# Performance work log

Hardware: AMD Instinct MI355X
Metric: run time of the kernel (lower is better)

## Reference

```python
import jax, jax.numpy as jnp
import numpy as np
jax.config.update("jax_enable_x64", True)  # hash math needs int64 like torch .long()

NUM_LEVELS = 16
BASE_RES = 16
LOG2_HASHMAP = 19
FEAT_DIM = 2
N_POINTS = 2097152
PRIMES = (1, 2654435761, 805459861)


def setup_inputs() -> dict:
    key = jax.random.key(0)
    k1, k2 = jax.random.split(key)
    xyz = jax.random.uniform(k1, (N_POINTS, 3), dtype=jnp.float32)
    # 16 hash tables of shape [2**19, 2], init randn * 0.1 as in the module
    tables = jax.random.normal(
        k2, (NUM_LEVELS, 2 ** LOG2_HASHMAP, FEAT_DIM), dtype=jnp.float32) * 0.1
    return {"xyz": xyz, "tables": tables}


def reference(xyz, tables):
    L, F = NUM_LEVELS, FEAT_DIM
    N = xyz.shape[0]
    grid_res = (BASE_RES * (2 ** jnp.arange(L, dtype=jnp.int64)))  # [L]
    # scale + truncate-to-int per level (xyz >= 0 so trunc == floor, matches .long())
    scaled = xyz[None, :, :] * grid_res[:, None, None].astype(xyz.dtype)  # [L, N, 3]
    idx = scaled.astype(jnp.int64)  # [L, N, 3]
    # spatial hash: (x*1) ^ (y*p1) ^ (z*p2) mod 2**19
    h = (idx[..., 0] * PRIMES[0]) ^ (idx[..., 1] * PRIMES[1]) ^ (idx[..., 2] * PRIMES[2])
    h = h % (1 << LOG2_HASHMAP)  # [L, N], non-negative
    # per-level gather from its own table
    feats = jax.vmap(lambda t, hh: t[hh])(tables, h)  # [L, N, F]
    # concat level features along last dim -> [N, L*F]
    return jnp.transpose(feats, (1, 0, 2)).reshape(N, L * F)
```

## Files before the change

### kernel.cpp

```cpp
#include <hip/hip_runtime.h>

#define NUM_LEVELS 16
#define LOG2_HASHMAP 19
#define TABLE_SIZE (1u << LOG2_HASHMAP)

typedef unsigned long long u64;

__global__ __launch_bounds__(256) void gather_kernel(
    const float* __restrict__ xyz,
    const float* __restrict__ tables,
    u64* __restrict__ ws,
    int n_points, int blocks_per_level)
{
    int b = blockIdx.x;
    int l = b / blocks_per_level;
    int n = (b - l * blocks_per_level) * 256 + threadIdx.x;
    if (n >= n_points) return;

    float x = xyz[n * 3 + 0];
    float y = xyz[n * 3 + 1];
    float z = xyz[n * 3 + 2];

    float res = (float)(16u << l);
    unsigned ix = (unsigned)(x * res);
    unsigned iy = (unsigned)(y * res);
    unsigned iz = (unsigned)(z * res);
    unsigned h = (ix ^ (iy * 2654435761u) ^ (iz * 805459861u)) & (TABLE_SIZE - 1u);

    u64 f = *((const u64*)tables + (((size_t)l << LOG2_HASHMAP) + h));
    __builtin_nontemporal_store(f, ws + (size_t)l * n_points + n);
}

__global__ __launch_bounds__(256) void transpose_kernel(
    const u64* __restrict__ ws,
    u64* __restrict__ out,
    int n_points)
{
    __shared__ u64 tile[128][NUM_LEVELS + 1];
    int n0 = blockIdx.x * 128;

    for (int i = threadIdx.x; i < 128 * NUM_LEVELS; i += 256) {
        int l = i >> 7;
        int n = i & 127;
        int gn = n0 + n;
        u64 v = (gn < n_points)
                  ? __builtin_nontemporal_load(ws + (size_t)l * n_points + gn)
                  : 0ull;
        tile[n][l] = v;
    }
    __syncthreads();

    for (int i = threadIdx.x; i < 128 * NUM_LEVELS; i += 256) {
        int n = i >> 4;
        int l = i & 15;
        if (n0 + n < n_points)
            __builtin_nontemporal_store(tile[n][l], out + (size_t)n0 * NUM_LEVELS + i);
    }
}

__global__ __launch_bounds__(256) void fused_kernel(
    const float* __restrict__ xyz,
    const float* __restrict__ tables,
    u64* __restrict__ out,
    int n_points)
{
    int tid = blockIdx.x * blockDim.x + threadIdx.x;
    int n = tid >> 4;
    int l = tid & 15;
    if (n >= n_points) return;
    float x = xyz[n * 3 + 0], y = xyz[n * 3 + 1], z = xyz[n * 3 + 2];
    float res = (float)(16u << l);
    unsigned ix = (unsigned)(x * res);
    unsigned iy = (unsigned)(y * res);
    unsigned iz = (unsigned)(z * res);
    unsigned h = (ix ^ (iy * 2654435761u) ^ (iz * 805459861u)) & (TABLE_SIZE - 1u);
    u64 f = *((const u64*)tables + (((size_t)l << LOG2_HASHMAP) + h));
    out[(size_t)n * NUM_LEVELS + l] = f;
}

extern "C" void kernel_launch(void* const* d_in, const int* in_sizes, int n_in,
                              void* d_out, int out_size, void* d_ws, size_t ws_size,
                              hipStream_t stream) {
    const float* xyz    = (const float*)d_in[0];
    const float* tables = (const float*)d_in[1];

    int n_points = in_sizes[0] / 3;
    size_t ws_needed = (size_t)n_points * NUM_LEVELS * sizeof(u64);

    if (ws_size >= ws_needed) {
        int blocks_per_level = (n_points + 255) / 256;
        int grid1 = blocks_per_level * NUM_LEVELS;
        gather_kernel<<<grid1, 256, 0, stream>>>(
            xyz, tables, (u64*)d_ws, n_points, blocks_per_level);

        int grid2 = (n_points + 127) / 128;
        transpose_kernel<<<grid2, 256, 0, stream>>>(
            (const u64*)d_ws, (u64*)d_out, n_points);
    } else {
        int total = n_points * NUM_LEVELS;
        int grid = (total + 255) / 256;
        fused_kernel<<<grid, 256, 0, stream>>>(xyz, tables, (u64*)d_out, n_points);
    }
}
```

Measured before the change: 327.7 us.

## Map hash levels to XCDs and batch eight gathers per thread

Reorders gather blocks so each of the 8 XCDs (round-robin block dispatch) handles one table level per phase, keeping each level's 4 MB table resident in that XCD's L2. Each thread now processes eight strided points and issues all eight table loads before any store, for more memory-level parallelism. The per-level scale is computed once at the finest resolution and shifted down, which drops a per-level float multiply. Risks: the XCD mapping assumes round-robin dispatch, and the fewer, larger blocks leave less parallelism to hide latency.

```diff
diff --git a/kernel.cpp b/kernel.cpp
--- a/kernel.cpp
+++ b/kernel.cpp
@@ -3,6 +3,7 @@
 #define NUM_LEVELS 16
 #define LOG2_HASHMAP 19
 #define TABLE_SIZE (1u << LOG2_HASHMAP)
+#define PPT 8
 
 typedef unsigned long long u64;
 
@@ -10,25 +11,47 @@
     const float* __restrict__ xyz,
     const float* __restrict__ tables,
     u64* __restrict__ ws,
-    int n_points, int blocks_per_level)
+    int n_points, int blocks_per_level, int stride_pts)
 {
-    int b = blockIdx.x;
-    int l = b / blocks_per_level;
-    int n = (b - l * blocks_per_level) * 256 + threadIdx.x;
-    if (n >= n_points) return;
+    int b     = blockIdx.x;
+    int xcd   = b & 7;
+    int j     = b >> 3;
+    int phase = (j >= blocks_per_level) ? 1 : 0;
+    int l     = xcd + (phase << 3);
+    int jj    = j - phase * blocks_per_level;
+    int base  = jj * 256 + (int)threadIdx.x;
 
-    float x = xyz[n * 3 + 0];
-    float y = xyz[n * 3 + 1];
-    float z = xyz[n * 3 + 2];
+    const u64* tbl = (const u64*)tables + ((size_t)l << LOG2_HASHMAP);
+    u64* wsl = ws + (size_t)l * n_points;
+    int shift = 15 - l;
 
-    float res = (float)(16u << l);
-    unsigned ix = (unsigned)(x * res);
-    unsigned iy = (unsigned)(y * res);
-    unsigned iz = (unsigned)(z * res);
-    unsigned h = (ix ^ (iy * 2654435761u) ^ (iz * 805459861u)) & (TABLE_SIZE - 1u);
+    unsigned hh[PPT];
+    int      nn[PPT];
+    bool     ok[PPT];
+#pragma unroll
+    for (int s = 0; s < PPT; ++s) {
+        int n = base + s * stride_pts;
+        nn[s] = n;
+        ok[s] = (n < n_points);
+        int ncl = ok[s] ? n : 0;
+        float x = xyz[ncl * 3 + 0];
+        float y = xyz[ncl * 3 + 1];
+        float z = xyz[ncl * 3 + 2];
+        unsigned wx = (unsigned)(x * 524288.0f) >> shift;
+        unsigned wy = (unsigned)(y * 524288.0f) >> shift;
+        unsigned wz = (unsigned)(z * 524288.0f) >> shift;
+        hh[s] = (wx ^ (wy * 2654435761u) ^ (wz * 805459861u)) & (TABLE_SIZE - 1u);
+    }
 
-    u64 f = *((const u64*)tables + (((size_t)l << LOG2_HASHMAP) + h));
-    __builtin_nontemporal_store(f, ws + (size_t)l * n_points + n);
+    u64 f[PPT];
+#pragma unroll
+    for (int s = 0; s < PPT; ++s)
+        f[s] = tbl[hh[s]];
+
+#pragma unroll
+    for (int s = 0; s < PPT; ++s)
+        if (ok[s])
+            __builtin_nontemporal_store(f[s], wsl + nn[s]);
 }
 
 __global__ __launch_bounds__(256) void transpose_kernel(
@@ -88,10 +111,11 @@
     size_t ws_needed = (size_t)n_points * NUM_LEVELS * sizeof(u64);
 
     if (ws_size >= ws_needed) {
-        int blocks_per_level = (n_points + 255) / 256;
+        int blocks_per_level = (n_points + 256 * PPT - 1) / (256 * PPT);
+        int stride_pts = blocks_per_level * 256;
         int grid1 = blocks_per_level * NUM_LEVELS;
         gather_kernel<<<grid1, 256, 0, stream>>>(
-            xyz, tables, (u64*)d_ws, n_points, blocks_per_level);
+            xyz, tables, (u64*)d_ws, n_points, blocks_per_level, stride_pts);
 
         int grid2 = (n_points + 127) / 128;
         transpose_kernel<<<grid2, 256, 0, stream>>>(
```

After: 319.3 us. -2.6%, faster.
